# Performance work log

Measured on AMD Instinct MI355X. Metric: run time of the kernel, lower is better.

Reference implementation:

```python
import jax, jax.numpy as jnp
import numpy as np

N, E, IN_DIM, OUT_DIM = 50000, 800000, 128, 128
NEG_SLOPE = 0.01  # F.leaky_relu default


def gcn_conv(x, W, b, src, dst, n_nodes):
    """PyG GCNConv: symmetric norm with self-loops, linear (no bias) -> aggregate -> +bias.
    Self-loop contribution added analytically (norm = deg_inv_sqrt[i]^2) instead of
    materializing an extended edge list."""
    h = x @ W.T  # [N, out]
    deg = jnp.zeros((n_nodes,), x.dtype).at[dst].add(1.0) + 1.0  # in-degree incl. self-loop
    dis = jax.lax.rsqrt(deg)  # deg^{-1/2}
    norm = dis[src] * dis[dst]  # [E]
    msgs = h[src] * norm[:, None]  # gather + scale, [E, out]
    agg = jax.ops.segment_sum(msgs, dst, num_segments=n_nodes)  # scatter-add
    agg = agg + h * (dis * dis)[:, None]  # self-loop messages
    return agg + b


def setup_inputs() -> dict:
    key = jax.random.key(0)
    ks = jax.random.split(key, 6)
    x = jax.random.normal(ks[0], (N, IN_DIM), jnp.float32)
    edge_index = jax.random.randint(ks[1], (2, E), 0, N, dtype=jnp.int32)
    batch = jnp.zeros((N,), jnp.int32)
    W1 = jax.random.normal(ks[2], (OUT_DIM, IN_DIM), jnp.float32) * (1.0 / np.sqrt(IN_DIM))
    b1 = jnp.zeros((OUT_DIM,), jnp.float32)
    W2 = jax.random.normal(ks[3], (OUT_DIM, OUT_DIM), jnp.float32) * (1.0 / np.sqrt(OUT_DIM))
    b2 = jnp.zeros((OUT_DIM,), jnp.float32)
    return {"x": x, "edge_index": edge_index, "batch": batch,
            "W1": W1, "b1": b1, "W2": W2, "b2": b2}


def reference(x, edge_index, batch, W1, b1, W2, b2):
    src, dst = edge_index[0], edge_index[1]
    n = x.shape[0]
    h = gcn_conv(x, W1, b1, src, dst, n)
    h = jax.nn.leaky_relu(h, NEG_SLOPE)
    # dropout is identity in eval mode (training=False)
    return gcn_conv(h, W2, b2, src, dst, n)
```

## Files before the change

### kernel.cpp

```cpp
#include <hip/hip_runtime.h>
#include <hip/hip_bf16.h>
#include <hip/hip_fp16.h>

#define DIM 128
#define NCHUNK 256
#define WLD 136

typedef unsigned short u16;
typedef unsigned int u32;
typedef __attribute__((ext_vector_type(8))) short bf16x8;
typedef __attribute__((ext_vector_type(4))) float f32x4;

__device__ __forceinline__ float bfbits2f(u16 u) {
    return __uint_as_float(((u32)u) << 16);
}
__device__ __forceinline__ u16 f2bf(float f) {
    __hip_bfloat16 b = __float2bfloat16(f);
    return *reinterpret_cast<u16*>(&b);
}
__device__ __forceinline__ u32 pack2bf(float lo, float hi) {
    return (u32)f2bf(lo) | ((u32)f2bf(hi) << 16);
}
__device__ __forceinline__ float h16tof(u16 u) {
    __half hh = *reinterpret_cast<__half*>(&u);
    return __half2float(hh);
}
__device__ __forceinline__ u16 ftoh16(float f) {
    __half hh = __float2half(f);
    return *reinterpret_cast<u16*>(&hh);
}

__device__ __forceinline__ int probe_flag_serial(const u16* __restrict__ x) {
    int weird = 0;
    for (int i = 0; i < 256; i += 2) {
        u16 v = x[i];
        int e = (v >> 7) & 0xff;
        if ((v & 0x7fff) != 0 && (e >= 133 || e <= 100)) weird++;
    }
    return (weird > 16) ? 1 : 0;
}

__global__ __launch_bounds__(256) void k_gemm_count(const void* __restrict__ in,
                                                    const void* __restrict__ W,
                                                    u16* __restrict__ h, int N,
                                                    const int* __restrict__ dst,
                                                    int* __restrict__ counts,
                                                    int* __restrict__ rank, int E,
                                                    int* __restrict__ flagp,
                                                    int gblk, int cblk) {
    const int bid = blockIdx.x;
    const int tid = threadIdx.x;

    if (bid & 1) {
        const int cid = bid >> 1;
        if (cid >= cblk) return;
        if (cid == 0 && tid == 0) *flagp = probe_flag_serial((const u16*)in);
        const int base = cid * 1024;
#pragma unroll
        for (int k = 0; k < 4; ++k) {
            int e = base + k * 256 + tid;
            if (e < E) rank[e] = atomicAdd(&counts[dst[e]], 1);
        }
        return;
    }

    const int gid = bid >> 1;
    if (gid >= gblk) return;

    __shared__ u16 Wsh[128 * WLD];
    __shared__ int flag_sh;
    if (tid == 0) flag_sh = 0;
    __syncthreads();
    if (tid < 128) {
        u16 v = ((const u16*)in)[tid * 2];
        int ex = (v >> 7) & 0xff;
        if ((v & 0x7fff) != 0 && (ex >= 133 || ex <= 100)) atomicAdd(&flag_sh, 1);
    }
    __syncthreads();
    const int flag = (flag_sh > 16) ? 1 : 0;
    const int n0 = gid * 64;

    if (flag) {
        const float* Wf = (const float*)W;
        for (int t = tid; t < 128 * 32; t += 256) {
            int r = t >> 5, c4 = (t & 31) * 4;
            float4 w = *(const float4*)(Wf + r * DIM + c4);
            uint2 pw = make_uint2(pack2bf(w.x, w.y), pack2bf(w.z, w.w));
            *(uint2*)(Wsh + r * WLD + c4) = pw;
        }
    } else {
        const u16* Wu = (const u16*)W;
        for (int t = tid; t < 128 * 16; t += 256) {
            int r = t >> 4, c8 = (t & 15) * 8;
            *(int4*)(Wsh + r * WLD + c8) = *(const int4*)(Wu + r * DIM + c8);
        }
    }

    const int wid = tid >> 6;
    const int lane = tid & 63;
    const int m_base = wid * 16;
    const int idx16 = lane & 15;
    const int koff = (lane >> 4) * 8;
    const int n = n0 + m_base + idx16;

    bf16x8 afrag[4];
    if (flag) {
        const float* xf = (const float*)in;
#pragma unroll
        for (int ks = 0; ks < 4; ++ks) {
            if (n < N) {
                const float* p = xf + (size_t)n * DIM + ks * 32 + koff;
                float4 a = *(const float4*)p;
                float4 b = *(const float4*)(p + 4);
                union { bf16x8 v8; u32 w[4]; } cv;
                cv.w[0] = pack2bf(a.x, a.y);
                cv.w[1] = pack2bf(a.z, a.w);
                cv.w[2] = pack2bf(b.x, b.y);
                cv.w[3] = pack2bf(b.z, b.w);
                afrag[ks] = cv.v8;
            } else {
                afrag[ks] = (bf16x8)0;
            }
        }
    } else {
        const u16* xu = (const u16*)in;
#pragma unroll
        for (int ks = 0; ks < 4; ++ks) {
            afrag[ks] = (n < N) ? *(const bf16x8*)(xu + (size_t)n * DIM + ks * 32 + koff)
                                : (bf16x8)0;
        }
    }
    __syncthreads();

    f32x4 acc[8];
#pragma unroll
    for (int ct = 0; ct < 8; ++ct) acc[ct] = (f32x4){0.f, 0.f, 0.f, 0.f};

#pragma unroll
    for (int ct = 0; ct < 8; ++ct) {
#pragma unroll
        for (int ks = 0; ks < 4; ++ks) {
            bf16x8 bfrag = *(const bf16x8*)(Wsh + (ct * 16 + idx16) * WLD + ks * 32 + koff);
            acc[ct] = __builtin_amdgcn_mfma_f32_16x16x32_bf16(afrag[ks], bfrag, acc[ct], 0, 0, 0);
        }
    }

    const int drow = (lane >> 4) * 4;
#pragma unroll
    for (int ct = 0; ct < 8; ++ct) {
#pragma unroll
        for (int r = 0; r < 4; ++r) {
            int row = n0 + m_base + drow + r;
            if (row < N) h[(size_t)row * DIM + ct * 16 + idx16] = f2bf(acc[ct][r]);
        }
    }
}

__global__ __launch_bounds__(256) void k_chunksum(const int* __restrict__ counts,
                                                  int* __restrict__ chunksum,
                                                  int N, int chunk) {
    __shared__ int r[256];
    int t = threadIdx.x, b = blockIdx.x;
    int idx = b * chunk + t;
    r[t] = (t < chunk && idx < N) ? counts[idx] + 1 : 0;
    __syncthreads();
    for (int off = 128; off > 0; off >>= 1) {
        if (t < off) r[t] += r[t + off];
        __syncthreads();
    }
    if (t == 0) chunksum[b] = r[0];
}

__global__ __launch_bounds__(256) void k_rowptr(const int* __restrict__ counts,
                                                const int* __restrict__ chunksum,
                                                int* __restrict__ rowptr,
                                                float* __restrict__ dis,
                                                u32* __restrict__ pay,
                                                int N, int chunk) {
    __shared__ int scb[256];
    __shared__ int sc[256];
    int t = threadIdx.x, b = blockIdx.x;

    int cs = chunksum[t];
    scb[t] = cs;
    __syncthreads();
    for (int off = 1; off < 256; off <<= 1) {
        int add = (t >= off) ? scb[t - off] : 0;
        __syncthreads();
        scb[t] += add;
        __syncthreads();
    }
    if (b == 0 && t == 0) rowptr[N] = scb[255];
    const int base = (b == 0) ? 0 : scb[b - 1];

    int idx = b * chunk + t;
    int v = (t < chunk && idx < N) ? counts[idx] + 1 : 0;
    sc[t] = v;
    __syncthreads();
    for (int off = 1; off < 256; off <<= 1) {
        int add = (t >= off) ? sc[t - off] : 0;
        __syncthreads();
        sc[t] += add;
        __syncthreads();
    }
    if (t < chunk && idx < N) {
        rowptr[idx] = base + sc[t] - v;
        float dv = rsqrtf((float)v);
        dis[idx] = dv;
        pay[idx] = ((u32)idx << 16) | (u32)ftoh16(dv);
    }
}

__global__ __launch_bounds__(256) void k_fill(const int* __restrict__ src,
                                              const int* __restrict__ dst,
                                              const int* __restrict__ rowptr,
                                              const int* __restrict__ rank,
                                              const u32* __restrict__ pay,
                                              u32* __restrict__ elist, int E, int N) {
    int e = blockIdx.x * blockDim.x + threadIdx.x;
    if (e < E) {
        elist[rowptr[dst[e]] + rank[e]] = pay[src[e]];
    } else if (e < E + N) {
        int d = e - E;
        elist[rowptr[d + 1] - 1] = pay[d];
    }
}

__global__ __launch_bounds__(256) void k_gemm(const void* __restrict__ in,
                                              const void* __restrict__ W,
                                              u16* __restrict__ h, int N,
                                              const int* __restrict__ flagp) {
    __shared__ u16 Wsh[128 * WLD];
    const int tid = threadIdx.x;
    const int flag = *flagp;
    const int n0 = blockIdx.x * 64;

    if (flag) {
        const float* Wf = (const float*)W;
        for (int t = tid; t < 128 * 32; t += 256) {
            int r = t >> 5, c4 = (t & 31) * 4;
            float4 w = *(const float4*)(Wf + r * DIM + c4);
            uint2 pw = make_uint2(pack2bf(w.x, w.y), pack2bf(w.z, w.w));
            *(uint2*)(Wsh + r * WLD + c4) = pw;
        }
    } else {
        const u16* Wu = (const u16*)W;
        for (int t = tid; t < 128 * 16; t += 256) {
            int r = t >> 4, c8 = (t & 15) * 8;
            *(int4*)(Wsh + r * WLD + c8) = *(const int4*)(Wu + r * DIM + c8);
        }
    }

    const int wid = tid >> 6;
    const int lane = tid & 63;
    const int m_base = wid * 16;
    const int idx16 = lane & 15;
    const int koff = (lane >> 4) * 8;
    const int n = n0 + m_base + idx16;

    bf16x8 afrag[4];
    const u16* xu = (const u16*)in;
#pragma unroll
    for (int ks = 0; ks < 4; ++ks) {
        afrag[ks] = (n < N) ? *(const bf16x8*)(xu + (size_t)n * DIM + ks * 32 + koff)
                            : (bf16x8)0;
    }
    __syncthreads();

    f32x4 acc[8];
#pragma unroll
    for (int ct = 0; ct < 8; ++ct) acc[ct] = (f32x4){0.f, 0.f, 0.f, 0.f};

#pragma unroll
    for (int ct = 0; ct < 8; ++ct) {
#pragma unroll
        for (int ks = 0; ks < 4; ++ks) {
            bf16x8 bfrag = *(const bf16x8*)(Wsh + (ct * 16 + idx16) * WLD + ks * 32 + koff);
            acc[ct] = __builtin_amdgcn_mfma_f32_16x16x32_bf16(afrag[ks], bfrag, acc[ct], 0, 0, 0);
        }
    }

    const int drow = (lane >> 4) * 4;
#pragma unroll
    for (int ct = 0; ct < 8; ++ct) {
#pragma unroll
        for (int r = 0; r < 4; ++r) {
            int row = n0 + m_base + drow + r;
            if (row < N) h[(size_t)row * DIM + ct * 16 + idx16] = f2bf(acc[ct][r]);
        }
    }
}

template <bool RELU, bool OUT_BF16>
__global__ __launch_bounds__(256) void k_agg(const u16* __restrict__ h,
                                             const float* __restrict__ dis,
                                             const int* __restrict__ rowptr,
                                             const u32* __restrict__ elist,
                                             const void* __restrict__ bias,
                                             void* __restrict__ out, int N,
                                             const int* __restrict__ flagp) {
    const int lane = threadIdx.x & 63;
    const int d = blockIdx.x * 4 + (threadIdx.x >> 6);
    if (d >= N) return;
    const int flag = *flagp;
    const int q  = lane >> 4;
    const int cb = (lane & 15) * 8;

    const int start = rowptr[d];
    const int end   = rowptr[d + 1];
    const int last  = end - 1;
    const float dd  = dis[d];

    float acc[8];
#pragma unroll
    for (int k = 0; k < 8; ++k) acc[k] = 0.f;

    for (int j = start; j < end; j += 16) {
        const int i0 = j + q, i1 = i0 + 4, i2 = i0 + 8, i3 = i0 + 12;
        const u32 e0 = elist[i0 <= last ? i0 : last];
        const u32 e1 = elist[i1 <= last ? i1 : last];
        const u32 e2 = elist[i2 <= last ? i2 : last];
        const u32 e3 = elist[i3 <= last ? i3 : last];
        const float w0 = (i0 <= last) ? h16tof((u16)(e0 & 0xffff)) : 0.f;
        const float w1 = (i1 <= last) ? h16tof((u16)(e1 & 0xffff)) : 0.f;
        const float w2 = (i2 <= last) ? h16tof((u16)(e2 & 0xffff)) : 0.f;
        const float w3 = (i3 <= last) ? h16tof((u16)(e3 & 0xffff)) : 0.f;
        const int4 r0 = *(const int4*)(h + ((size_t)(e0 >> 16)) * DIM + cb);
        const int4 r1 = *(const int4*)(h + ((size_t)(e1 >> 16)) * DIM + cb);
        const int4 r2 = *(const int4*)(h + ((size_t)(e2 >> 16)) * DIM + cb);
        const int4 r3 = *(const int4*)(h + ((size_t)(e3 >> 16)) * DIM + cb);
        const u32 v0[4] = {(u32)r0.x, (u32)r0.y, (u32)r0.z, (u32)r0.w};
        const u32 v1[4] = {(u32)r1.x, (u32)r1.y, (u32)r1.z, (u32)r1.w};
        const u32 v2[4] = {(u32)r2.x, (u32)r2.y, (u32)r2.z, (u32)r2.w};
        const u32 v3[4] = {(u32)r3.x, (u32)r3.y, (u32)r3.z, (u32)r3.w};
#pragma unroll
        for (int k = 0; k < 4; ++k) {
            acc[2 * k]     = fmaf(bfbits2f((u16)(v0[k] & 0xffff)), w0, acc[2 * k]);
            acc[2 * k + 1] = fmaf(bfbits2f((u16)(v0[k] >> 16)),    w0, acc[2 * k + 1]);
        }
#pragma unroll
        for (int k = 0; k < 4; ++k) {
            acc[2 * k]     = fmaf(bfbits2f((u16)(v1[k] & 0xffff)), w1, acc[2 * k]);
            acc[2 * k + 1] = fmaf(bfbits2f((u16)(v1[k] >> 16)),    w1, acc[2 * k + 1]);
        }
#pragma unroll
        for (int k = 0; k < 4; ++k) {
            acc[2 * k]     = fmaf(bfbits2f((u16)(v2[k] & 0xffff)), w2, acc[2 * k]);
            acc[2 * k + 1] = fmaf(bfbits2f((u16)(v2[k] >> 16)),    w2, acc[2 * k + 1]);
        }
#pragma unroll
        for (int k = 0; k < 4; ++k) {
            acc[2 * k]     = fmaf(bfbits2f((u16)(v3[k] & 0xffff)), w3, acc[2 * k]);
            acc[2 * k + 1] = fmaf(bfbits2f((u16)(v3[k] >> 16)),    w3, acc[2 * k + 1]);
        }
    }

#pragma unroll
    for (int k = 0; k < 8; ++k) {
        acc[k] += __shfl_xor(acc[k], 16, 64);
        acc[k] += __shfl_xor(acc[k], 32, 64);
    }

    if (q != 0) return;

    float res[8];
#pragma unroll
    for (int k = 0; k < 8; ++k) res[k] = acc[k] * dd;
    if (flag) {
        const float* bf = (const float*)bias;
#pragma unroll
        for (int k = 0; k < 8; ++k) res[k] += bf[cb + k];
    } else {
        const u16* bu = (const u16*)bias;
#pragma unroll
        for (int k = 0; k < 8; ++k) res[k] += bfbits2f(bu[cb + k]);
    }
    if (RELU) {
#pragma unroll
        for (int k = 0; k < 8; ++k) res[k] = res[k] > 0.f ? res[k] : 0.01f * res[k];
    }
    if (OUT_BF16) {
        u32 pk[4];
#pragma unroll
        for (int k = 0; k < 4; ++k) pk[k] = pack2bf(res[2 * k], res[2 * k + 1]);
        *(int4*)((u16*)out + (size_t)d * DIM + cb) = make_int4(pk[0], pk[1], pk[2], pk[3]);
    } else {
        float* op = (float*)out + (size_t)d * DIM + cb;
        *(float4*)op       = make_float4(res[0], res[1], res[2], res[3]);
        *(float4*)(op + 4) = make_float4(res[4], res[5], res[6], res[7]);
    }
}

extern "C" void kernel_launch(void* const* d_in, const int* in_sizes, int n_in,
                              void* d_out, int out_size, void* d_ws, size_t ws_size,
                              hipStream_t stream) {
    const void* x  = d_in[0];
    const int*  ei = (const int*)d_in[1];
    const void* W1 = d_in[3];
    const void* b1 = d_in[4];
    const void* W2 = d_in[5];
    const void* b2 = d_in[6];

    const int N = in_sizes[0] / DIM;
    const int E = in_sizes[1] / 2;
    const int* src = ei;
    const int* dst = ei + E;
    const int chunk = (N + NCHUNK - 1) / NCHUNK;

    char* ws = (char*)d_ws;
    size_t o = 0;
    int*   flagp    = (int*)(ws + o);   o += 256;
    float* dis      = (float*)(ws + o); o += (((size_t)N * 4 + 255) & ~(size_t)255);
    int*   counts   = (int*)(ws + o);   o += (((size_t)N * 4 + 255) & ~(size_t)255);
    int*   rowptr   = (int*)(ws + o);   o += (((size_t)(N + 1) * 4 + 255) & ~(size_t)255);
    u32*   pay      = (u32*)(ws + o);   o += (((size_t)N * 4 + 255) & ~(size_t)255);
    int*   chunksum = (int*)(ws + o);   o += 1024;
    int*   rank     = (int*)(ws + o);   o += (((size_t)E * 4 + 255) & ~(size_t)255);
    u32*   elist    = (u32*)(ws + o);   o += (((size_t)(E + N) * 4 + 255) & ~(size_t)255);
    u16*   h        = (u16*)(ws + o);

    const int gblk = (N + 63) / 64;
    const int cblk = (E + 1023) / 1024;
    const int fused_nb = 2 * (gblk > cblk ? gblk : cblk);
    const int fblk = (E + N + 255) / 256;
    const int ablk = (N + 3) / 4;

    u16* act = (u16*)d_out;

    hipMemsetAsync(counts, 0, (size_t)N * 4, stream);
    k_gemm_count<<<fused_nb, 256, 0, stream>>>(x, W1, h, N, dst, counts, rank, E,
                                               flagp, gblk, cblk);
    k_chunksum<<<NCHUNK, 256, 0, stream>>>(counts, chunksum, N, chunk);
    k_rowptr<<<NCHUNK, 256, 0, stream>>>(counts, chunksum, rowptr, dis, pay, N, chunk);
    k_fill<<<fblk, 256, 0, stream>>>(src, dst, rowptr, rank, pay, elist, E, N);

    k_agg<true, true><<<ablk, 256, 0, stream>>>(h, dis, rowptr, elist, b1, act, N, flagp);

    k_gemm<<<gblk, 256, 0, stream>>>(act, W2, h, N, flagp);
    k_agg<false, false><<<ablk, 256, 0, stream>>>(h, dis, rowptr, elist, b2, d_out, N, flagp);
}
```

Baseline: 218.9 us.

## Split feature matrix into two 64-column halves and aggregate each half separately

The GEMM kernels now write h as two separate N×64 bf16 planes instead of one N×128 matrix. Each aggregation pass runs twice, once per half, with 8 edges processed per wavefront step instead of 4. The intent is to halve the gathered working set per pass (about 6.4MB instead of 12.8MB) so random row gathers hit cache better. The cost is reading the edge list twice and two extra kernel launches.

```diff
diff --git a/kernel.cpp b/kernel.cpp
--- a/kernel.cpp
+++ b/kernel.cpp
@@ -42,7 +42,8 @@
 
 __global__ __launch_bounds__(256) void k_gemm_count(const void* __restrict__ in,
                                                     const void* __restrict__ W,
-                                                    u16* __restrict__ h, int N,
+                                                    u16* __restrict__ h0,
+                                                    u16* __restrict__ h1, int N,
                                                     const int* __restrict__ dst,
                                                     int* __restrict__ counts,
                                                     int* __restrict__ rank, int E,
@@ -148,10 +149,12 @@
     const int drow = (lane >> 4) * 4;
 #pragma unroll
     for (int ct = 0; ct < 8; ++ct) {
+        u16* hp = (ct < 4) ? h0 : h1;
+        const int pcol = (ct * 16 + idx16) & 63;
 #pragma unroll
         for (int r = 0; r < 4; ++r) {
             int row = n0 + m_base + drow + r;
-            if (row < N) h[(size_t)row * DIM + ct * 16 + idx16] = f2bf(acc[ct][r]);
+            if (row < N) hp[(size_t)row * 64 + pcol] = f2bf(acc[ct][r]);
         }
     }
 }
@@ -228,7 +231,8 @@
 
 __global__ __launch_bounds__(256) void k_gemm(const void* __restrict__ in,
                                               const void* __restrict__ W,
-                                              u16* __restrict__ h, int N,
+                                              u16* __restrict__ h0,
+                                              u16* __restrict__ h1, int N,
                                               const int* __restrict__ flagp) {
     __shared__ u16 Wsh[128 * WLD];
     const int tid = threadIdx.x;
@@ -283,28 +287,30 @@
     const int drow = (lane >> 4) * 4;
 #pragma unroll
     for (int ct = 0; ct < 8; ++ct) {
+        u16* hp = (ct < 4) ? h0 : h1;
+        const int pcol = (ct * 16 + idx16) & 63;
 #pragma unroll
         for (int r = 0; r < 4; ++r) {
             int row = n0 + m_base + drow + r;
-            if (row < N) h[(size_t)row * DIM + ct * 16 + idx16] = f2bf(acc[ct][r]);
+            if (row < N) hp[(size_t)row * 64 + pcol] = f2bf(acc[ct][r]);
         }
     }
 }
 
 template <bool RELU, bool OUT_BF16>
-__global__ __launch_bounds__(256) void k_agg(const u16* __restrict__ h,
+__global__ __launch_bounds__(256) void k_agg(const u16* __restrict__ hp,
                                              const float* __restrict__ dis,
                                              const int* __restrict__ rowptr,
                                              const u32* __restrict__ elist,
                                              const void* __restrict__ bias,
-                                             void* __restrict__ out, int N,
+                                             void* __restrict__ out, int N, int co,
                                              const int* __restrict__ flagp) {
     const int lane = threadIdx.x & 63;
     const int d = blockIdx.x * 4 + (threadIdx.x >> 6);
     if (d >= N) return;
     const int flag = *flagp;
-    const int q  = lane >> 4;
-    const int cb = (lane & 15) * 8;
+    const int sub = lane >> 3;
+    const int cb  = (lane & 7) * 8;
 
     const int start = rowptr[d];
     const int end   = rowptr[d + 1];
@@ -315,8 +321,8 @@
 #pragma unroll
     for (int k = 0; k < 8; ++k) acc[k] = 0.f;
 
-    for (int j = start; j < end; j += 16) {
-        const int i0 = j + q, i1 = i0 + 4, i2 = i0 + 8, i3 = i0 + 12;
+    for (int j = start; j < end; j += 32) {
+        const int i0 = j + sub, i1 = i0 + 8, i2 = i0 + 16, i3 = i0 + 24;
         const u32 e0 = elist[i0 <= last ? i0 : last];
         const u32 e1 = elist[i1 <= last ? i1 : last];
         const u32 e2 = elist[i2 <= last ? i2 : last];
@@ -325,10 +331,10 @@
         const float w1 = (i1 <= last) ? h16tof((u16)(e1 & 0xffff)) : 0.f;
         const float w2 = (i2 <= last) ? h16tof((u16)(e2 & 0xffff)) : 0.f;
         const float w3 = (i3 <= last) ? h16tof((u16)(e3 & 0xffff)) : 0.f;
-        const int4 r0 = *(const int4*)(h + ((size_t)(e0 >> 16)) * DIM + cb);
-        const int4 r1 = *(const int4*)(h + ((size_t)(e1 >> 16)) * DIM + cb);
-        const int4 r2 = *(const int4*)(h + ((size_t)(e2 >> 16)) * DIM + cb);
-        const int4 r3 = *(const int4*)(h + ((size_t)(e3 >> 16)) * DIM + cb);
+        const int4 r0 = *(const int4*)(hp + ((size_t)(e0 >> 16)) * 64 + cb);
+        const int4 r1 = *(const int4*)(hp + ((size_t)(e1 >> 16)) * 64 + cb);
+        const int4 r2 = *(const int4*)(hp + ((size_t)(e2 >> 16)) * 64 + cb);
+        const int4 r3 = *(const int4*)(hp + ((size_t)(e3 >> 16)) * 64 + cb);
         const u32 v0[4] = {(u32)r0.x, (u32)r0.y, (u32)r0.z, (u32)r0.w};
         const u32 v1[4] = {(u32)r1.x, (u32)r1.y, (u32)r1.z, (u32)r1.w};
         const u32 v2[4] = {(u32)r2.x, (u32)r2.y, (u32)r2.z, (u32)r2.w};
@@ -357,11 +363,12 @@
 
 #pragma unroll
     for (int k = 0; k < 8; ++k) {
+        acc[k] += __shfl_xor(acc[k], 8, 64);
         acc[k] += __shfl_xor(acc[k], 16, 64);
         acc[k] += __shfl_xor(acc[k], 32, 64);
     }
 
-    if (q != 0) return;
+    if (sub != 0) return;
 
     float res[8];
 #pragma unroll
@@ -369,11 +376,11 @@
     if (flag) {
         const float* bf = (const float*)bias;
 #pragma unroll
-        for (int k = 0; k < 8; ++k) res[k] += bf[cb + k];
+        for (int k = 0; k < 8; ++k) res[k] += bf[co + cb + k];
     } else {
         const u16* bu = (const u16*)bias;
 #pragma unroll
-        for (int k = 0; k < 8; ++k) res[k] += bfbits2f(bu[cb + k]);
+        for (int k = 0; k < 8; ++k) res[k] += bfbits2f(bu[co + cb + k]);
     }
     if (RELU) {
 #pragma unroll
@@ -383,9 +390,9 @@
         u32 pk[4];
 #pragma unroll
         for (int k = 0; k < 4; ++k) pk[k] = pack2bf(res[2 * k], res[2 * k + 1]);
-        *(int4*)((u16*)out + (size_t)d * DIM + cb) = make_int4(pk[0], pk[1], pk[2], pk[3]);
+        *(int4*)((u16*)out + (size_t)d * DIM + co + cb) = make_int4(pk[0], pk[1], pk[2], pk[3]);
     } else {
-        float* op = (float*)out + (size_t)d * DIM + cb;
+        float* op = (float*)out + (size_t)d * DIM + co + cb;
         *(float4*)op       = make_float4(res[0], res[1], res[2], res[3]);
         *(float4*)(op + 4) = make_float4(res[4], res[5], res[6], res[7]);
     }
@@ -417,7 +424,8 @@
     int*   chunksum = (int*)(ws + o);   o += 1024;
     int*   rank     = (int*)(ws + o);   o += (((size_t)E * 4 + 255) & ~(size_t)255);
     u32*   elist    = (u32*)(ws + o);   o += (((size_t)(E + N) * 4 + 255) & ~(size_t)255);
-    u16*   h        = (u16*)(ws + o);
+    u16*   h0       = (u16*)(ws + o);   o += (((size_t)N * 64 * 2 + 255) & ~(size_t)255);
+    u16*   h1       = (u16*)(ws + o);   o += (((size_t)N * 64 * 2 + 255) & ~(size_t)255);
 
     const int gblk = (N + 63) / 64;
     const int cblk = (E + 1023) / 1024;
@@ -428,14 +436,16 @@
     u16* act = (u16*)d_out;
 
     hipMemsetAsync(counts, 0, (size_t)N * 4, stream);
-    k_gemm_count<<<fused_nb, 256, 0, stream>>>(x, W1, h, N, dst, counts, rank, E,
+    k_gemm_count<<<fused_nb, 256, 0, stream>>>(x, W1, h0, h1, N, dst, counts, rank, E,
                                                flagp, gblk, cblk);
     k_chunksum<<<NCHUNK, 256, 0, stream>>>(counts, chunksum, N, chunk);
     k_rowptr<<<NCHUNK, 256, 0, stream>>>(counts, chunksum, rowptr, dis, pay, N, chunk);
     k_fill<<<fblk, 256, 0, stream>>>(src, dst, rowptr, rank, pay, elist, E, N);
 
-    k_agg<true, true><<<ablk, 256, 0, stream>>>(h, dis, rowptr, elist, b1, act, N, flagp);
-
-    k_gemm<<<gblk, 256, 0, stream>>>(act, W2, h, N, flagp);
-    k_agg<false, false><<<ablk, 256, 0, stream>>>(h, dis, rowptr, elist, b2, d_out, N, flagp);
-}
+    k_agg<true, true><<<ablk, 256, 0, stream>>>(h0, dis, rowptr, elist, b1, act, N, 0, flagp);
+    k_agg<true, true><<<ablk, 256, 0, stream>>>(h1, dis, rowptr, elist, b1, act, N, 64, flagp);
+
+    k_gemm<<<gblk, 256, 0, stream>>>(act, W2, h0, h1, N, flagp);
+    k_agg<false, false><<<ablk, 256, 0, stream>>>(h0, dis, rowptr, elist, b2, d_out, N, 0, flagp);
+    k_agg<false, false><<<ablk, 256, 0, stream>>>(h1, dis, rowptr, elist, b2, d_out, N, 64, flagp);
+}
```

Result: slower. 243.2 us (+11.1%).
